# Optimization experiments

Hardware: AMD Instinct MI355X
Metric: run time of the kernel (lower is better)

## Reference

```python
import jax, jax.numpy as jnp
import numpy as np

N, E = 16384, 262144
IN, H, OUT = 128, 256, 256
L, HEADS = 4, 8
OC = H // HEADS  # 32, also MHA head_dim
B, NB = 64, 256  # graphs, nodes per graph (N = B*NB, equal-size graphs)


def _ln(x, g, b, eps=1e-5):
    m = x.mean(-1, keepdims=True)
    v = ((x - m) ** 2).mean(-1, keepdims=True)
    return (x - m) / jnp.sqrt(v + eps) * g + b


def setup_inputs() -> dict:
    key = jax.random.key(0)
    ks = iter(jax.random.split(key, 40))
    r = lambda *s: jax.random.normal(next(ks), s, jnp.float32) * 0.05
    return dict(
        x=jax.random.normal(next(ks), (N, IN), jnp.float32),
        edge_index=jax.random.randint(next(ks), (2, E), 0, N),
        wi=r(IN, H), bi=r(H),
        wg=r(L, H, H), asrc=r(L, HEADS, OC), adst=r(L, HEADS, OC), bg=r(L, H),
        g1=jnp.ones((L, H)), b1=jnp.zeros((L, H)),
        inw=r(L, 3 * H, H), inb=r(L, 3 * H), ow=r(L, H, H), ob=r(L, H),
        g2=jnp.ones((L, H)), b2=jnp.zeros((L, H)),
        mw1=r(L, H, 2 * H), mb1=r(L, 2 * H), mw2=r(L, 2 * H, H), mb2=r(L, H),
        g3=jnp.ones((L, H)), b3=jnp.zeros((L, H)),
        gf=jnp.ones(H), bf=jnp.zeros(H),
        wo=r(H, OUT), bo=r(OUT),
    )


def reference(x, edge_index, wi, bi, wg, asrc, adst, bg, g1, b1, inw, inb,
              ow, ob, g2, b2, mw1, mb1, mw2, mb2, g3, b3, gf, bf, wo, bo):
    src, dst = edge_index[0], edge_index[1]
    x = jax.nn.relu(x @ wi + bi)  # [N, H]
    for i in range(L):
        # ---- GATConv (local MPNN), eval mode (no dropout) ----
        xw = (x @ wg[i]).reshape(N, HEADS, OC)
        a = (xw * asrc[i]).sum(-1)[src] + (xw * adst[i]).sum(-1)[dst]  # [E, HEADS]
        a = jax.nn.leaky_relu(a, 0.2)
        amax = jax.ops.segment_max(a, dst, num_segments=N)
        ae = jnp.exp(a - amax[dst])
        asum = jax.ops.segment_sum(ae, dst, num_segments=N)
        attn = ae / asum[dst]  # edge softmax per destination node
        h = jax.ops.segment_sum(attn[:, :, None] * xw[src], dst, num_segments=N)
        h = h.reshape(N, H) + bg[i]
        h = _ln(h + x, g1[i], b1[i])  # GPSConv local branch + residual + norm1
        # ---- global MultiheadAttention over dense batch (equal-size graphs) ----
        xd = x.reshape(B, NB, H)
        qkv = xd @ inw[i].T + inb[i]
        q, k, v = jnp.split(qkv, 3, axis=-1)
        q = q.reshape(B, NB, HEADS, OC).transpose(0, 2, 1, 3)
        k = k.reshape(B, NB, HEADS, OC).transpose(0, 2, 1, 3)
        v = v.reshape(B, NB, HEADS, OC).transpose(0, 2, 1, 3)
        p = jax.nn.softmax(jnp.einsum('bhqd,bhkd->bhqk', q, k) / jnp.sqrt(jnp.float32(OC)), axis=-1)
        o = jnp.einsum('bhqk,bhkd->bhqd', p, v).transpose(0, 2, 1, 3).reshape(B, NB, H)
        o = (o @ ow[i].T + ob[i]).reshape(N, H)
        h2 = _ln(o + x, g2[i], b2[i])  # global branch + residual + norm2
        out = h + h2
        out = out + (jax.nn.relu(out @ mw1[i] + mb1[i]) @ mw2[i] + mb2[i])  # MLP residual
        x = _ln(out, g3[i], b3[i])  # norm3
    x = _ln(x, gf, bf)
    return x @ wo + bo
```

## Files before the change

### kernel.cpp

```cpp
#include <hip/hip_runtime.h>
#include <hip/hip_bf16.h>

#define NNODES 16384
#define NEDGES 262144
#define IND    128
#define HD     256
#define OUTDIM 256
#define LAYERS 4
#define NHEADS 8
#define OCD    32
#define NGRAPH 64
#define NBATCH 256
#define XQSTR  1024

typedef __hip_bfloat16 bf16;
typedef __attribute__((ext_vector_type(8))) short bf16x8;
typedef __attribute__((ext_vector_type(4))) short s16x4;
typedef __attribute__((ext_vector_type(4))) float f32x4;

__device__ __forceinline__ short bfbits(float v) {
    bf16 h = __float2bfloat16(v);
    return *(short*)&h;
}
__device__ __forceinline__ float b2f(short s) {
    return __uint_as_float(((unsigned)(unsigned short)s) << 16);
}

__device__ __forceinline__ void gload_lds16(const short* g, short* l) {
    __builtin_amdgcn_global_load_lds(
        (const __attribute__((address_space(1))) void*)g,
        (__attribute__((address_space(3))) void*)l, 16, 0, 0);
}

__global__ void cvt_kernel(const float* __restrict__ in, short* __restrict__ out, int n)
{
    int i = blockIdx.x * blockDim.x + threadIdx.x;
    if (i < n) out[i] = bfbits(in[i]);
}

__global__ void transpose_cvt_kernel(const float* __restrict__ in, short* __restrict__ out,
                                     int K, int N)
{
    int i = blockIdx.x * blockDim.x + threadIdx.x;
    if (i >= K * N) return;
    const float* ip = in + (size_t)blockIdx.y * K * N;
    short* op = out + (size_t)blockIdx.y * K * N;
    int k = i / N, n = i % N;
    op[(size_t)n * K + k] = bfbits(ip[i]);
}

__global__ void build_wcomb_kernel(const float* __restrict__ inw, const float* __restrict__ wg,
                                   short* __restrict__ wcomb)
{
    int i = blockIdx.x * blockDim.x + threadIdx.x;
    int l = i >> 18, r = (i >> 8) & 1023, k = i & 255;
    float v;
    if (r < 768) v = inw[(size_t)l * 768 * 256 + r * 256 + k];
    else         v = wg[(size_t)l * 256 * 256 + k * 256 + (r - 768)];
    wcomb[i] = bfbits(v);
}

__global__ void build_cbias_kernel(const float* __restrict__ inb, float* __restrict__ cbias)
{
    int i = blockIdx.x * blockDim.x + threadIdx.x;
    int l = i >> 10, c = i & 1023;
    cbias[i] = (c < 768) ? inb[l * 768 + c] : 0.f;
}

__global__ void hist_kernel(const int* __restrict__ dst, int* __restrict__ cnt)
{
    int e = blockIdx.x * blockDim.x + threadIdx.x;
    if (e < NEDGES) atomicAdd(&cnt[dst[e]], 1);
}

__global__ void scan_kernel(const int* __restrict__ cnt, int* __restrict__ row_ptr)
{
    __shared__ int part[256];
    int t = threadIdx.x;
    const int PER = NNODES / 256;
    int base = t * PER;
    int s = 0;
    for (int i = 0; i < PER; i++) s += cnt[base + i];
    part[t] = s;
    __syncthreads();
    for (int off = 1; off < 256; off <<= 1) {
        int v = (t >= off) ? part[t - off] : 0;
        __syncthreads();
        part[t] += v;
        __syncthreads();
    }
    int run = (t == 0) ? 0 : part[t - 1];
    for (int i = 0; i < PER; i++) { row_ptr[base + i] = run; run += cnt[base + i]; }
    if (t == 255) row_ptr[NNODES] = run;
}

__global__ void scatter_kernel(const int* __restrict__ src, const int* __restrict__ dst,
                               const int* __restrict__ row_ptr, int* __restrict__ fill,
                               int* __restrict__ srcs)
{
    int e = blockIdx.x * blockDim.x + threadIdx.x;
    if (e >= NEDGES) return;
    int d = dst[e];
    int pos = row_ptr[d] + atomicAdd(&fill[d], 1);
    srcs[pos] = src[e];
}

__global__ void gat_scores_kernel(const short* __restrict__ xw16,
                                  const float* __restrict__ asrc, const float* __restrict__ adst,
                                  float* __restrict__ ssrc, float* __restrict__ sdst)
{
    int i = blockIdx.x * blockDim.x + threadIdx.x;
    if (i >= NNODES * NHEADS) return;
    int n = i >> 3, h = i & 7;
    const bf16x8* xr = (const bf16x8*)(xw16 + (size_t)n * XQSTR + h * OCD);
    float s1 = 0.f, s2 = 0.f;
#pragma unroll
    for (int g = 0; g < 4; g++) {
        bf16x8 v8 = xr[g];
#pragma unroll
        for (int j = 0; j < 8; j++) {
            float v = b2f(v8[j]);
            int d = g * 8 + j;
            s1 += v * asrc[h * OCD + d];
            s2 += v * adst[h * OCD + d];
        }
    }
    ssrc[i] = s1;
    sdst[i] = s2;
}

__global__ __launch_bounds__(256)
void gat_agg_ln_kernel(const int* __restrict__ row_ptr, const int* __restrict__ srcs,
                       const float* __restrict__ ssrc, const float* __restrict__ sdst,
                       const short* __restrict__ xw16, const float* __restrict__ xcur,
                       const float* __restrict__ colbias, const float* __restrict__ gamma,
                       const float* __restrict__ beta, float* __restrict__ out)
{
    int wave = threadIdx.x >> 6, lane = threadIdx.x & 63;
    int n = blockIdx.x * 4 + wave;
    int c0 = lane << 2;
    int h = c0 >> 5;
    int start = row_ptr[n];
    int deg = row_ptr[n + 1] - start;
    float sd = sdst[n * NHEADS + h];

    float ax = 0.f, ay = 0.f, az = 0.f, aw = 0.f, l = 0.f;
    int j = 0;
    for (; j + 4 <= deg; j += 4) {
        int e0 = srcs[start + j + 0], e1 = srcs[start + j + 1];
        int e2 = srcs[start + j + 2], e3 = srcs[start + j + 3];
        s16x4 r0 = *(const s16x4*)&xw16[(size_t)e0 * XQSTR + c0];
        s16x4 r1 = *(const s16x4*)&xw16[(size_t)e1 * XQSTR + c0];
        s16x4 r2 = *(const s16x4*)&xw16[(size_t)e2 * XQSTR + c0];
        s16x4 r3 = *(const s16x4*)&xw16[(size_t)e3 * XQSTR + c0];
        float a0 = ssrc[e0 * NHEADS + h] + sd; a0 = a0 > 0.f ? a0 : 0.2f * a0;
        float a1 = ssrc[e1 * NHEADS + h] + sd; a1 = a1 > 0.f ? a1 : 0.2f * a1;
        float a2 = ssrc[e2 * NHEADS + h] + sd; a2 = a2 > 0.f ? a2 : 0.2f * a2;
        float a3 = ssrc[e3 * NHEADS + h] + sd; a3 = a3 > 0.f ? a3 : 0.2f * a3;
        float p0 = __expf(a0), p1 = __expf(a1), p2 = __expf(a2), p3 = __expf(a3);
        l += (p0 + p1) + (p2 + p3);
        ax += p0 * b2f(r0[0]) + p1 * b2f(r1[0]) + p2 * b2f(r2[0]) + p3 * b2f(r3[0]);
        ay += p0 * b2f(r0[1]) + p1 * b2f(r1[1]) + p2 * b2f(r2[1]) + p3 * b2f(r3[1]);
        az += p0 * b2f(r0[2]) + p1 * b2f(r1[2]) + p2 * b2f(r2[2]) + p3 * b2f(r3[2]);
        aw += p0 * b2f(r0[3]) + p1 * b2f(r1[3]) + p2 * b2f(r2[3]) + p3 * b2f(r3[3]);
    }
    for (; j < deg; j++) {
        int e0 = srcs[start + j];
        s16x4 r0 = *(const s16x4*)&xw16[(size_t)e0 * XQSTR + c0];
        float a0 = ssrc[e0 * NHEADS + h] + sd; a0 = a0 > 0.f ? a0 : 0.2f * a0;
        float p0 = __expf(a0);
        l += p0;
        ax += p0 * b2f(r0[0]); ay += p0 * b2f(r0[1]);
        az += p0 * b2f(r0[2]); aw += p0 * b2f(r0[3]);
    }
    float invl = deg ? 1.f / l : 0.f;
    size_t base = (size_t)n * HD + c0;
    float4 x4 = *(const float4*)&xcur[base];
    float4 cb = *(const float4*)&colbias[c0];
    float4 v;
    v.x = ax * invl + x4.x + cb.x;
    v.y = ay * invl + x4.y + cb.y;
    v.z = az * invl + x4.z + cb.z;
    v.w = aw * invl + x4.w + cb.w;
    float s = v.x + v.y + v.z + v.w;
    float q = v.x * v.x + v.y * v.y + v.z * v.z + v.w * v.w;
#pragma unroll
    for (int off = 1; off < 64; off <<= 1) {
        s += __shfl_xor(s, off);
        q += __shfl_xor(q, off);
    }
    float mean = s * (1.f / HD);
    float var  = fmaxf(q * (1.f / HD) - mean * mean, 0.f);
    float inv  = rsqrtf(var + 1e-5f);
    float4 g  = *(const float4*)&gamma[c0];
    float4 bt = *(const float4*)&beta[c0];
    float4 y;
    y.x = (v.x - mean) * inv * g.x + bt.x;
    y.y = (v.y - mean) * inv * g.y + bt.y;
    y.z = (v.z - mean) * inv * g.z + bt.z;
    y.w = (v.w - mean) * inv * g.w + bt.w;
    *(float4*)&out[base] = y;
}

#define GBM 128
#define GBK 32

template<int TN>
__global__ __launch_bounds__(256)
void gemm_mfma_kernel(const short* __restrict__ A16, const short* __restrict__ B16,
                      const float* __restrict__ bias, const float* __restrict__ resid,
                      float* __restrict__ Cf, short* __restrict__ C16,
                      int M, int Nc, int K, int relu)
{
    constexpr int NTF = TN / 32;
    __shared__ short As[GBM * GBK];
    __shared__ short Bs[TN * GBK];
    int tid = threadIdx.x;
    int wid = tid >> 6, lane = tid & 63;
    int quad = lane >> 4, l16 = lane & 15;
    int wm = wid >> 1, wn = wid & 1;
    int rowBase = blockIdx.y * GBM;
    int colBase = blockIdx.x * TN;

    f32x4 acc[4][NTF];
#pragma unroll
    for (int mt = 0; mt < 4; mt++)
#pragma unroll
        for (int nt = 0; nt < NTF; nt++) acc[mt][nt] = (f32x4)(0.f);

    int ar  = tid >> 2;
    int akq = (tid & 3) * 8;

    const short* Ag0 = &A16[(size_t)(rowBase + ar) * K + akq];
    const short* Ag1 = &A16[(size_t)(rowBase + ar + 64) * K + akq];
    const short* Bg0 = &B16[(size_t)(colBase + ar) * K + akq];
    const short* Bg1 = (TN == 128) ? &B16[(size_t)(colBase + ar + 64) * K + akq] : nullptr;
    short* AsW0 = As + wid * 512;
    short* AsW1 = As + 64 * GBK + wid * 512;
    short* BsW0 = Bs + wid * 512;
    short* BsW1 = Bs + 64 * GBK + wid * 512;

    for (int k0 = 0; k0 < K; k0 += GBK) {
        gload_lds16(Ag0 + k0, AsW0);
        gload_lds16(Ag1 + k0, AsW1);
        gload_lds16(Bg0 + k0, BsW0);
        if (TN == 128) gload_lds16(Bg1 + k0, BsW1);
        __syncthreads();
        bf16x8 aF[4], bF[NTF];
#pragma unroll
        for (int mt = 0; mt < 4; mt++)
            aF[mt] = *(bf16x8*)&As[(wm * 64 + mt * 16 + l16) * GBK + quad * 8];
#pragma unroll
        for (int nt = 0; nt < NTF; nt++)
            bF[nt] = *(bf16x8*)&Bs[(wn * (TN / 2) + nt * 16 + l16) * GBK + quad * 8];
#pragma unroll
        for (int mt = 0; mt < 4; mt++)
#pragma unroll
            for (int nt = 0; nt < NTF; nt++)
                acc[mt][nt] = __builtin_amdgcn_mfma_f32_16x16x32_bf16(
                    bF[nt], aF[mt], acc[mt][nt], 0, 0, 0);
        __syncthreads();
    }

#pragma unroll
    for (int mt = 0; mt < 4; mt++) {
        int row = rowBase + wm * 64 + mt * 16 + l16;
#pragma unroll
        for (int nt = 0; nt < NTF; nt++) {
            int col0 = colBase + wn * (TN / 2) + nt * 16 + quad * 4;
            f32x4 v = acc[mt][nt];
            if (bias) {
                float4 b4 = *(const float4*)&bias[col0];
                v[0] += b4.x; v[1] += b4.y; v[2] += b4.z; v[3] += b4.w;
            }
            if (resid) {
                float4 r4 = *(const float4*)&resid[(size_t)row * Nc + col0];
                v[0] += r4.x; v[1] += r4.y; v[2] += r4.z; v[3] += r4.w;
            }
            if (relu) {
                v[0] = fmaxf(v[0], 0.f); v[1] = fmaxf(v[1], 0.f);
                v[2] = fmaxf(v[2], 0.f); v[3] = fmaxf(v[3], 0.f);
            }
            if (Cf) {
                float4 o; o.x = v[0]; o.y = v[1]; o.z = v[2]; o.w = v[3];
                *(float4*)&Cf[(size_t)row * Nc + col0] = o;
            }
            if (C16) {
                s16x4 o;
                o[0] = bfbits(v[0]); o[1] = bfbits(v[1]);
                o[2] = bfbits(v[2]); o[3] = bfbits(v[3]);
                *(s16x4*)&C16[(size_t)row * Nc + col0] = o;
            }
        }
    }
}

__global__ __launch_bounds__(256)
void gemm_ln_kernel(const short* __restrict__ A16, const short* __restrict__ B16,
                    const float* __restrict__ bias, const float* __restrict__ resid,
                    const float* __restrict__ gamma, const float* __restrict__ beta,
                    const float* __restrict__ postadd,
                    float* __restrict__ outf, short* __restrict__ out16, int K)
{
    __shared__ short As[GBM * GBK];
    __shared__ short Bs[256 * GBK];
    __shared__ float sred_s[2][GBM];
    __shared__ float sred_q[2][GBM];
    int tid = threadIdx.x;
    int wid = tid >> 6, lane = tid & 63;
    int quad = lane >> 4, l16 = lane & 15;
    int wm = wid >> 1, wn = wid & 1;
    int rowBase = blockIdx.y * GBM;

    f32x4 acc[4][8];
#pragma unroll
    for (int mt = 0; mt < 4; mt++)
#pragma unroll
        for (int nt = 0; nt < 8; nt++) acc[mt][nt] = (f32x4)(0.f);

    int ar  = tid >> 2;
    int akq = (tid & 3) * 8;

    const short* Ag0 = &A16[(size_t)(rowBase + ar) * K + akq];
    const short* Ag1 = &A16[(size_t)(rowBase + ar + 64) * K + akq];
    const short* Bg0 = &B16[(size_t)(ar) * K + akq];
    const short* Bg1 = &B16[(size_t)(ar + 64) * K + akq];
    const short* Bg2 = &B16[(size_t)(ar + 128) * K + akq];
    const short* Bg3 = &B16[(size_t)(ar + 192) * K + akq];
    short* AsW0 = As + wid * 512;
    short* AsW1 = As + 64 * GBK + wid * 512;
    short* BsW0 = Bs + wid * 512;
    short* BsW1 = Bs + 64 * GBK + wid * 512;
    short* BsW2 = Bs + 128 * GBK + wid * 512;
    short* BsW3 = Bs + 192 * GBK + wid * 512;

    for (int k0 = 0; k0 < K; k0 += GBK) {
        gload_lds16(Ag0 + k0, AsW0);
        gload_lds16(Ag1 + k0, AsW1);
        gload_lds16(Bg0 + k0, BsW0);
        gload_lds16(Bg1 + k0, BsW1);
        gload_lds16(Bg2 + k0, BsW2);
        gload_lds16(Bg3 + k0, BsW3);
        __syncthreads();
        bf16x8 aF[4], bF[8];
#pragma unroll
        for (int mt = 0; mt < 4; mt++)
            aF[mt] = *(bf16x8*)&As[(wm * 64 + mt * 16 + l16) * GBK + quad * 8];
#pragma unroll
        for (int nt = 0; nt < 8; nt++)
            bF[nt] = *(bf16x8*)&Bs[(wn * 128 + nt * 16 + l16) * GBK + quad * 8];
#pragma unroll
        for (int mt = 0; mt < 4; mt++)
#pragma unroll
            for (int nt = 0; nt < 8; nt++)
                acc[mt][nt] = __builtin_amdgcn_mfma_f32_16x16x32_bf16(
                    bF[nt], aF[mt], acc[mt][nt], 0, 0, 0);
        __syncthreads();
    }

#pragma unroll
    for (int mt = 0; mt < 4; mt++) {
        int row = rowBase + wm * 64 + mt * 16 + l16;
        float s = 0.f, q = 0.f;
#pragma unroll
        for (int nt = 0; nt < 8; nt++) {
            int col0 = wn * 128 + nt * 16 + quad * 4;
            f32x4 v = acc[mt][nt];
            float4 b4 = *(const float4*)&bias[col0];
            float4 r4 = *(const float4*)&resid[(size_t)row * HD + col0];
            v[0] += b4.x + r4.x; v[1] += b4.y + r4.y;
            v[2] += b4.z + r4.z; v[3] += b4.w + r4.w;
            acc[mt][nt] = v;
            s += (v[0] + v[1]) + (v[2] + v[3]);
            q += (v[0] * v[0] + v[1] * v[1]) + (v[2] * v[2] + v[3] * v[3]);
        }
        s += __shfl_xor(s, 16); s += __shfl_xor(s, 32);
        q += __shfl_xor(q, 16); q += __shfl_xor(q, 32);
        if (quad == 0) {
            sred_s[wn][wm * 64 + mt * 16 + l16] = s;
            sred_q[wn][wm * 64 + mt * 16 + l16] = q;
        }
    }
    __syncthreads();
#pragma unroll
    for (int mt = 0; mt < 4; mt++) {
        int rowl = wm * 64 + mt * 16 + l16;
        int row = rowBase + rowl;
        float s = sred_s[0][rowl] + sred_s[1][rowl];
        float q = sred_q[0][rowl] + sred_q[1][rowl];
        float mean = s * (1.f / HD);
        float var  = fmaxf(q * (1.f / HD) - mean * mean, 0.f);
        float inv  = rsqrtf(var + 1e-5f);
#pragma unroll
        for (int nt = 0; nt < 8; nt++) {
            int col0 = wn * 128 + nt * 16 + quad * 4;
            f32x4 v = acc[mt][nt];
            float4 g4 = *(const float4*)&gamma[col0];
            float4 bt = *(const float4*)&beta[col0];
            float4 y;
            y.x = (v[0] - mean) * inv * g4.x + bt.x;
            y.y = (v[1] - mean) * inv * g4.y + bt.y;
            y.z = (v[2] - mean) * inv * g4.z + bt.z;
            y.w = (v[3] - mean) * inv * g4.w + bt.w;
            if (postadd) {
                float4 p4 = *(const float4*)&postadd[(size_t)row * HD + col0];
                y.x += p4.x; y.y += p4.y; y.z += p4.z; y.w += p4.w;
            }
            *(float4*)&outf[(size_t)row * HD + col0] = y;
            s16x4 o;
            o[0] = bfbits(y.x); o[1] = bfbits(y.y); o[2] = bfbits(y.z); o[3] = bfbits(y.w);
            *(s16x4*)&out16[(size_t)row * HD + col0] = o;
        }
    }
}

__global__ __launch_bounds__(256)
void ln4_kernel(const float* __restrict__ in, const float* __restrict__ res,
                const float* __restrict__ gamma, const float* __restrict__ beta,
                const float* __restrict__ postadd,
                float* __restrict__ outf, short* __restrict__ out16)
{
    int wave = threadIdx.x >> 6, lane = threadIdx.x & 63;
    int row = blockIdx.x * 4 + wave;
    size_t base = (size_t)row * HD + lane * 4;
    float4 v = *(const float4*)&in[base];
    if (res) {
        float4 r = *(const float4*)&res[base];
        v.x += r.x; v.y += r.y; v.z += r.z; v.w += r.w;
    }
    float s = v.x + v.y + v.z + v.w;
    float q = v.x * v.x + v.y * v.y + v.z * v.z + v.w * v.w;
#pragma unroll
    for (int off = 1; off < 64; off <<= 1) {
        s += __shfl_xor(s, off);
        q += __shfl_xor(q, off);
    }
    float mean = s * (1.f / HD);
    float var  = fmaxf(q * (1.f / HD) - mean * mean, 0.f);
    float inv  = rsqrtf(var + 1e-5f);
    float4 g  = *(const float4*)&gamma[lane * 4];
    float4 bt = *(const float4*)&beta[lane * 4];
    float4 y;
    y.x = (v.x - mean) * inv * g.x + bt.x;
    y.y = (v.y - mean) * inv * g.y + bt.y;
    y.z = (v.z - mean) * inv * g.z + bt.z;
    y.w = (v.w - mean) * inv * g.w + bt.w;
    if (postadd) {
        float4 p = *(const float4*)&postadd[base];
        y.x += p.x; y.y += p.y; y.z += p.z; y.w += p.w;
    }
    if (outf) *(float4*)&outf[base] = y;
    if (out16) {
        s16x4 o;
        o[0] = bfbits(y.x); o[1] = bfbits(y.y); o[2] = bfbits(y.z); o[3] = bfbits(y.w);
        *(s16x4*)&out16[base] = o;
    }
}

#define PSTR 72
__global__ __launch_bounds__(256)
void mha_mfma_kernel(const short* __restrict__ qkv16, short* __restrict__ o16)
{
    __shared__ short smem[4 * 64 * PSTR + 32 * PSTR];
    short* VT = smem + 4 * 64 * PSTR;

    int b = blockIdx.x, h = blockIdx.y;
    int tid = threadIdx.x;
    int wid = tid >> 6, lane = tid & 63;
    int quad = lane >> 4, l16 = lane & 15;
    int base = b * NBATCH;
    int qrow0 = wid * 64;
    short* Pme = smem + wid * 64 * PSTR;

    const float scale2 = 0.17677669529663687f * 1.4426950408889634f;

    bf16x8 qA[4];
#pragma unroll
    for (int mt = 0; mt < 4; mt++)
        qA[mt] = *(const bf16x8*)&qkv16[(size_t)(base + qrow0 + mt * 16 + l16) * XQSTR + h * 32 + quad * 8];

    f32x4 accO[4][2];
#pragma unroll
    for (int mt = 0; mt < 4; mt++)
#pragma unroll
        for (int dt = 0; dt < 2; dt++) accO[mt][dt] = (f32x4)(0.f);
    float lsum[4][4];
#pragma unroll
    for (int mt = 0; mt < 4; mt++)
#pragma unroll
        for (int r = 0; r < 4; r++) lsum[mt][r] = 0.f;

    for (int c = 0; c < 4; c++) {
        __syncthreads();
        {
            int key = tid >> 2, dq = (tid & 3) * 8;
            bf16x8 v = *(const bf16x8*)&qkv16[(size_t)(base + c * 64 + key) * XQSTR + 512 + h * 32 + dq];
#pragma unroll
            for (int j = 0; j < 8; j++) VT[(dq + j) * PSTR + key] = v[j];
        }
        __syncthreads();
        bf16x8 kB[4];
#pragma unroll
        for (int kt = 0; kt < 4; kt++)
            kB[kt] = *(const bf16x8*)&qkv16[(size_t)(base + c * 64 + kt * 16 + l16) * XQSTR + 256 + h * 32 + quad * 8];
#pragma unroll
        for (int mt = 0; mt < 4; mt++) {
#pragma unroll
            for (int kt = 0; kt < 4; kt++) {
                f32x4 s = __builtin_amdgcn_mfma_f32_16x16x32_bf16(qA[mt], kB[kt], (f32x4)(0.f), 0, 0, 0);
#pragma unroll
                for (int r = 0; r < 4; r++) {
                    float p = exp2f(s[r] * scale2);
                    lsum[mt][r] += p;
                    Pme[(mt * 16 + quad * 4 + r) * PSTR + kt * 16 + l16] = bfbits(p);
                }
            }
        }
        __syncthreads();
#pragma unroll
        for (int mt = 0; mt < 4; mt++) {
#pragma unroll
            for (int ks = 0; ks < 2; ks++) {
                bf16x8 pA = *(bf16x8*)&Pme[(mt * 16 + l16) * PSTR + ks * 32 + quad * 8];
#pragma unroll
                for (int dt = 0; dt < 2; dt++) {
                    bf16x8 vB = *(bf16x8*)&VT[(dt * 16 + l16) * PSTR + ks * 32 + quad * 8];
                    accO[mt][dt] = __builtin_amdgcn_mfma_f32_16x16x32_bf16(pA, vB, accO[mt][dt], 0, 0, 0);
                }
            }
        }
    }
#pragma unroll
    for (int mt = 0; mt < 4; mt++)
#pragma unroll
        for (int r = 0; r < 4; r++) {
            float v = lsum[mt][r];
            v += __shfl_xor(v, 1);
            v += __shfl_xor(v, 2);
            v += __shfl_xor(v, 4);
            v += __shfl_xor(v, 8);
            lsum[mt][r] = v;
        }
#pragma unroll
    for (int mt = 0; mt < 4; mt++)
#pragma unroll
        for (int dt = 0; dt < 2; dt++)
#pragma unroll
            for (int r = 0; r < 4; r++) {
                int row = base + qrow0 + mt * 16 + quad * 4 + r;
                int col = h * 32 + dt * 16 + l16;
                o16[(size_t)row * HD + col] = bfbits(accO[mt][dt][r] / lsum[mt][r]);
            }
}

extern "C" void kernel_launch(void* const* d_in, const int* in_sizes, int n_in,
                              void* d_out, int out_size, void* d_ws, size_t ws_size,
                              hipStream_t stream)
{
    const float* x0   = (const float*)d_in[0];
    const int*   ei   = (const int*)d_in[1];
    const float* wi   = (const float*)d_in[2];
    const float* bi   = (const float*)d_in[3];
    const float* wg   = (const float*)d_in[4];
    const float* asrc = (const float*)d_in[5];
    const float* adst = (const float*)d_in[6];
    const float* bg   = (const float*)d_in[7];
    const float* g1   = (const float*)d_in[8];
    const float* b1   = (const float*)d_in[9];
    const float* inw  = (const float*)d_in[10];
    const float* inb  = (const float*)d_in[11];
    const float* ow   = (const float*)d_in[12];
    const float* ob   = (const float*)d_in[13];
    const float* g2   = (const float*)d_in[14];
    const float* b2   = (const float*)d_in[15];
    const float* mw1  = (const float*)d_in[16];
    const float* mb1  = (const float*)d_in[17];
    const float* mw2  = (const float*)d_in[18];
    const float* mb2  = (const float*)d_in[19];
    const float* g3   = (const float*)d_in[20];
    const float* b3   = (const float*)d_in[21];
    const float* gf   = (const float*)d_in[22];
    const float* bf_  = (const float*)d_in[23];
    const float* wo   = (const float*)d_in[24];
    const float* bo   = (const float*)d_in[25];

    const int* srcI = ei;
    const int* dstI = ei + NEDGES;

    const size_t NH = (size_t)NNODES * HD;
    float* ws   = (float*)d_ws;
    float* xcur = ws;
    float* xw   = xcur + NH;
    float* hbuf = xw + NH;
    float* obuf = hbuf + NH;
    float* qkvb = obuf + NH;
    int*   srcs    = (int*)(qkvb + 3 * NH);
    int*   row_ptr = srcs + NEDGES;
    int*   cnt     = row_ptr + NNODES + 1;
    int*   fill    = cnt + NNODES;
    float* ssrc    = (float*)(fill + NNODES);
    float* sdst    = ssrc + (size_t)NNODES * NHEADS;
    short* xq16   = (short*)qkvb;
    short* x016   = (short*)(sdst + (size_t)NNODES * NHEADS);
    short* xcur16 = x016 + (size_t)NNODES * IND;
    short* b16a   = xcur16 + NH;
    short* hid16  = b16a + NH;
    short* wi_t  = hid16 + 2 * NH;
    short* wcomb = wi_t + (size_t)HD * IND;
    short* ow_c  = wcomb + (size_t)LAYERS * 1024 * HD;
    short* mw1_t = ow_c + (size_t)LAYERS * HD * HD;
    short* mw2_t = mw1_t + (size_t)LAYERS * HD * 2 * HD;
    short* wo_t  = mw2_t + (size_t)LAYERS * 2 * HD * HD;
    float* cbias = (float*)(wo_t + (size_t)HD * OUTDIM);

    const int T = 256;
    const int nNH = NNODES * NHEADS;

    cvt_kernel<<<(NNODES * IND + T - 1) / T, T, 0, stream>>>(x0, x016, NNODES * IND);
    transpose_cvt_kernel<<<dim3((IND * HD + T - 1) / T, 1), T, 0, stream>>>(wi, wi_t, IND, HD);
    build_wcomb_kernel<<<(LAYERS * 1024 * HD) / T, T, 0, stream>>>(inw, wg, wcomb);
    build_cbias_kernel<<<(LAYERS * 1024) / T, T, 0, stream>>>(inb, cbias);
    cvt_kernel<<<(LAYERS * HD * HD + T - 1) / T, T, 0, stream>>>(ow, ow_c, LAYERS * HD * HD);
    transpose_cvt_kernel<<<dim3((HD * 2 * HD + T - 1) / T, LAYERS), T, 0, stream>>>(mw1, mw1_t, HD, 2 * HD);
    transpose_cvt_kernel<<<dim3((2 * HD * HD + T - 1) / T, LAYERS), T, 0, stream>>>(mw2, mw2_t, 2 * HD, HD);
    transpose_cvt_kernel<<<dim3((HD * OUTDIM + T - 1) / T, 1), T, 0, stream>>>(wo, wo_t, HD, OUTDIM);

    hipMemsetAsync(cnt, 0, NNODES * sizeof(int), stream);
    hipMemsetAsync(fill, 0, NNODES * sizeof(int), stream);
    hist_kernel<<<(NEDGES + T - 1) / T, T, 0, stream>>>(dstI, cnt);
    scan_kernel<<<1, 256, 0, stream>>>(cnt, row_ptr);
    scatter_kernel<<<(NEDGES + T - 1) / T, T, 0, stream>>>(srcI, dstI, row_ptr, fill, srcs);

    gemm_mfma_kernel<64><<<dim3(HD / 64, NNODES / GBM), 256, 0, stream>>>(
        x016, wi_t, bi, nullptr, xcur, xcur16, NNODES, HD, IND, 1);

    for (int i = 0; i < LAYERS; i++) {
        const float* asrc_i = asrc + (size_t)i * NHEADS * OCD;
        const float* adst_i = adst + (size_t)i * NHEADS * OCD;
        const float* bg_i   = bg + (size_t)i * HD;
        const float* g1_i   = g1 + (size_t)i * HD;
        const float* b1_i   = b1 + (size_t)i * HD;
        const float* ob_i   = ob + (size_t)i * HD;
        const float* g2_i   = g2 + (size_t)i * HD;
        const float* b2_i   = b2 + (size_t)i * HD;
        const float* mb1_i  = mb1 + (size_t)i * 2 * HD;
        const float* mb2_i  = mb2 + (size_t)i * HD;
        const float* g3_i   = g3 + (size_t)i * HD;
        const float* b3_i   = b3 + (size_t)i * HD;
        const short* wcomb_i = wcomb + (size_t)i * 1024 * HD;
        const float* cbias_i = cbias + (size_t)i * 1024;
        const short* ow_ci  = ow_c + (size_t)i * HD * HD;
        const short* mw1_ti = mw1_t + (size_t)i * HD * 2 * HD;
        const short* mw2_ti = mw2_t + (size_t)i * 2 * HD * HD;

        gemm_mfma_kernel<128><<<dim3(1024 / 128, NNODES / GBM), 256, 0, stream>>>(
            xcur16, wcomb_i, cbias_i, nullptr, nullptr, xq16, NNODES, 1024, HD, 0);

        gat_scores_kernel<<<(nNH + T - 1) / T, T, 0, stream>>>(xq16 + 768, asrc_i, adst_i, ssrc, sdst);
        gat_agg_ln_kernel<<<NNODES / 4, 256, 0, stream>>>(
            row_ptr, srcs, ssrc, sdst, xq16 + 768, xcur, bg_i, g1_i, b1_i, hbuf);

        mha_mfma_kernel<<<dim3(NGRAPH, NHEADS), 256, 0, stream>>>(xq16, b16a);
        gemm_ln_kernel<<<dim3(1, NNODES / GBM), 256, 0, stream>>>(
            b16a, ow_ci, ob_i, xcur, g2_i, b2_i, hbuf, obuf, b16a, HD);

        gemm_mfma_kernel<128><<<dim3(2 * HD / 128, NNODES / GBM), 256, 0, stream>>>(
            b16a, mw1_ti, mb1_i, nullptr, nullptr, hid16, NNODES, 2 * HD, HD, 1);
        gemm_ln_kernel<<<dim3(1, NNODES / GBM), 256, 0, stream>>>(
            hid16, mw2_ti, mb2_i, obuf, g3_i, b3_i, nullptr, xcur, xcur16, 2 * HD);
    }

    ln4_kernel<<<NNODES / 4, 256, 0, stream>>>(xcur, nullptr, gf, bf_, nullptr, nullptr, b16a);
    gemm_mfma_kernel<64><<<dim3(OUTDIM / 64, NNODES / GBM), 256, 0, stream>>>(
        b16a, wo_t, bo, nullptr, (float*)d_out, nullptr, NNODES, OUTDIM, HD, 0);
}
```

Baseline: 892.7 us.

## Shrink gemm_ln row tile to 64 and fuse weight prep into one kernel

The GEMM+LayerNorm kernel now uses 64-row tiles in which each wave owns 16 full rows across all 256 columns. Row statistics are reduced within a wave by shuffles, so the shared-memory reduction and its extra barrier go away, and the grid doubles from 128 to 256 blocks for better CU occupancy. The separate conversion, transpose and memset launches are also merged into a single prep kernel to cut launch overhead. The trade-off is less B-tile reuse per block, since each block reloads the whole weight matrix for half as many rows.

```diff
diff --git a/kernel.cpp b/kernel.cpp
--- a/kernel.cpp
+++ b/kernel.cpp
@@ -32,39 +32,67 @@
         (__attribute__((address_space(3))) void*)l, 16, 0, 0);
 }
 
-__global__ void cvt_kernel(const float* __restrict__ in, short* __restrict__ out, int n)
+#define PREP_TOTAL (32768 + NNODES*IND + IND*HD + LAYERS*1024*HD + LAYERS*1024 \
+                    + LAYERS*HD*HD + LAYERS*HD*2*HD + LAYERS*2*HD*HD + HD*OUTDIM)
+__global__ void prep_kernel(const float* __restrict__ x0, const float* __restrict__ wi,
+                            const float* __restrict__ inw, const float* __restrict__ wg,
+                            const float* __restrict__ inb, const float* __restrict__ ow,
+                            const float* __restrict__ mw1, const float* __restrict__ mw2,
+                            const float* __restrict__ wo,
+                            short* __restrict__ x016, short* __restrict__ wi_t,
+                            short* __restrict__ wcomb, float* __restrict__ cbias,
+                            short* __restrict__ ow_c, short* __restrict__ mw1_t,
+                            short* __restrict__ mw2_t, short* __restrict__ wo_t,
+                            int* __restrict__ cnt, int* __restrict__ fill)
 {
     int i = blockIdx.x * blockDim.x + threadIdx.x;
-    if (i < n) out[i] = bfbits(in[i]);
-}
-
-__global__ void transpose_cvt_kernel(const float* __restrict__ in, short* __restrict__ out,
-                                     int K, int N)
-{
-    int i = blockIdx.x * blockDim.x + threadIdx.x;
-    if (i >= K * N) return;
-    const float* ip = in + (size_t)blockIdx.y * K * N;
-    short* op = out + (size_t)blockIdx.y * K * N;
-    int k = i / N, n = i % N;
-    op[(size_t)n * K + k] = bfbits(ip[i]);
-}
-
-__global__ void build_wcomb_kernel(const float* __restrict__ inw, const float* __restrict__ wg,
-                                   short* __restrict__ wcomb)
-{
-    int i = blockIdx.x * blockDim.x + threadIdx.x;
-    int l = i >> 18, r = (i >> 8) & 1023, k = i & 255;
-    float v;
-    if (r < 768) v = inw[(size_t)l * 768 * 256 + r * 256 + k];
-    else         v = wg[(size_t)l * 256 * 256 + k * 256 + (r - 768)];
-    wcomb[i] = bfbits(v);
-}
-
-__global__ void build_cbias_kernel(const float* __restrict__ inb, float* __restrict__ cbias)
-{
-    int i = blockIdx.x * blockDim.x + threadIdx.x;
-    int l = i >> 10, c = i & 1023;
-    cbias[i] = (c < 768) ? inb[l * 768 + c] : 0.f;
+    if (i < 32768) {
+        if (i < NNODES) cnt[i] = 0; else fill[i - NNODES] = 0;
+        return;
+    }
+    i -= 32768;
+    if (i < NNODES * IND) { x016[i] = bfbits(x0[i]); return; }
+    i -= NNODES * IND;
+    if (i < IND * HD) {
+        int k = i / HD, n = i % HD;
+        wi_t[n * IND + k] = bfbits(wi[i]);
+        return;
+    }
+    i -= IND * HD;
+    if (i < LAYERS * 1024 * HD) {
+        int l = i >> 18, r = (i >> 8) & 1023, k = i & 255;
+        float v = (r < 768) ? inw[(size_t)l * 768 * 256 + r * 256 + k]
+                            : wg[(size_t)l * 256 * 256 + k * 256 + (r - 768)];
+        wcomb[i] = bfbits(v);
+        return;
+    }
+    i -= LAYERS * 1024 * HD;
+    if (i < LAYERS * 1024) {
+        int l = i >> 10, c = i & 1023;
+        cbias[i] = (c < 768) ? inb[l * 768 + c] : 0.f;
+        return;
+    }
+    i -= LAYERS * 1024;
+    if (i < LAYERS * HD * HD) { ow_c[i] = bfbits(ow[i]); return; }
+    i -= LAYERS * HD * HD;
+    if (i < LAYERS * HD * 2 * HD) {
+        int l = i / (HD * 2 * HD), r = i % (HD * 2 * HD);
+        int k = r / (2 * HD), n = r % (2 * HD);
+        mw1_t[(size_t)l * HD * 2 * HD + n * HD + k] = bfbits(mw1[i]);
+        return;
+    }
+    i -= LAYERS * HD * 2 * HD;
+    if (i < LAYERS * 2 * HD * HD) {
+        int l = i / (2 * HD * HD), r = i % (2 * HD * HD);
+        int k = r / HD, n = r % HD;
+        mw2_t[(size_t)l * 2 * HD * HD + n * 2 * HD + k] = bfbits(mw2[i]);
+        return;
+    }
+    i -= LAYERS * 2 * HD * HD;
+    if (i < HD * OUTDIM) {
+        int k = i / OUTDIM, n = i % OUTDIM;
+        wo_t[n * HD + k] = bfbits(wo[i]);
+    }
 }
 
 __global__ void hist_kernel(const int* __restrict__ dst, int* __restrict__ cnt)
@@ -302,115 +330,85 @@
                     const float* __restrict__ postadd,
                     float* __restrict__ outf, short* __restrict__ out16, int K)
 {
-    __shared__ short As[GBM * GBK];
+    __shared__ short As[64 * GBK];
     __shared__ short Bs[256 * GBK];
-    __shared__ float sred_s[2][GBM];
-    __shared__ float sred_q[2][GBM];
     int tid = threadIdx.x;
     int wid = tid >> 6, lane = tid & 63;
     int quad = lane >> 4, l16 = lane & 15;
-    int wm = wid >> 1, wn = wid & 1;
-    int rowBase = blockIdx.y * GBM;
-
-    f32x4 acc[4][8];
-#pragma unroll
-    for (int mt = 0; mt < 4; mt++)
-#pragma unroll
-        for (int nt = 0; nt < 8; nt++) acc[mt][nt] = (f32x4)(0.f);
+    int rowBase = blockIdx.y * 64;
+
+    f32x4 acc[16];
+#pragma unroll
+    for (int nt = 0; nt < 16; nt++) acc[nt] = (f32x4)(0.f);
 
     int ar  = tid >> 2;
     int akq = (tid & 3) * 8;
 
-    const short* Ag0 = &A16[(size_t)(rowBase + ar) * K + akq];
-    const short* Ag1 = &A16[(size_t)(rowBase + ar + 64) * K + akq];
+    const short* Ag  = &A16[(size_t)(rowBase + ar) * K + akq];
     const short* Bg0 = &B16[(size_t)(ar) * K + akq];
     const short* Bg1 = &B16[(size_t)(ar + 64) * K + akq];
     const short* Bg2 = &B16[(size_t)(ar + 128) * K + akq];
     const short* Bg3 = &B16[(size_t)(ar + 192) * K + akq];
-    short* AsW0 = As + wid * 512;
-    short* AsW1 = As + 64 * GBK + wid * 512;
+    short* AsW  = As + wid * 512;
     short* BsW0 = Bs + wid * 512;
     short* BsW1 = Bs + 64 * GBK + wid * 512;
     short* BsW2 = Bs + 128 * GBK + wid * 512;
     short* BsW3 = Bs + 192 * GBK + wid * 512;
 
     for (int k0 = 0; k0 < K; k0 += GBK) {
-        gload_lds16(Ag0 + k0, AsW0);
-        gload_lds16(Ag1 + k0, AsW1);
+        gload_lds16(Ag + k0, AsW);
         gload_lds16(Bg0 + k0, BsW0);
         gload_lds16(Bg1 + k0, BsW1);
         gload_lds16(Bg2 + k0, BsW2);
         gload_lds16(Bg3 + k0, BsW3);
         __syncthreads();
-        bf16x8 aF[4], bF[8];
-#pragma unroll
-        for (int mt = 0; mt < 4; mt++)
-            aF[mt] = *(bf16x8*)&As[(wm * 64 + mt * 16 + l16) * GBK + quad * 8];
-#pragma unroll
-        for (int nt = 0; nt < 8; nt++)
-            bF[nt] = *(bf16x8*)&Bs[(wn * 128 + nt * 16 + l16) * GBK + quad * 8];
-#pragma unroll
-        for (int mt = 0; mt < 4; mt++)
-#pragma unroll
-            for (int nt = 0; nt < 8; nt++)
-                acc[mt][nt] = __builtin_amdgcn_mfma_f32_16x16x32_bf16(
-                    bF[nt], aF[mt], acc[mt][nt], 0, 0, 0);
-        __syncthreads();
-    }
-
-#pragma unroll
-    for (int mt = 0; mt < 4; mt++) {
-        int row = rowBase + wm * 64 + mt * 16 + l16;
-        float s = 0.f, q = 0.f;
-#pragma unroll
-        for (int nt = 0; nt < 8; nt++) {
-            int col0 = wn * 128 + nt * 16 + quad * 4;
-            f32x4 v = acc[mt][nt];
-            float4 b4 = *(const float4*)&bias[col0];
-            float4 r4 = *(const float4*)&resid[(size_t)row * HD + col0];
-            v[0] += b4.x + r4.x; v[1] += b4.y + r4.y;
-            v[2] += b4.z + r4.z; v[3] += b4.w + r4.w;
-            acc[mt][nt] = v;
-            s += (v[0] + v[1]) + (v[2] + v[3]);
-            q += (v[0] * v[0] + v[1] * v[1]) + (v[2] * v[2] + v[3] * v[3]);
-        }
-        s += __shfl_xor(s, 16); s += __shfl_xor(s, 32);
-        q += __shfl_xor(q, 16); q += __shfl_xor(q, 32);
-        if (quad == 0) {
-            sred_s[wn][wm * 64 + mt * 16 + l16] = s;
-            sred_q[wn][wm * 64 + mt * 16 + l16] = q;
-        }
-    }
-    __syncthreads();
-#pragma unroll
-    for (int mt = 0; mt < 4; mt++) {
-        int rowl = wm * 64 + mt * 16 + l16;
-        int row = rowBase + rowl;
-        float s = sred_s[0][rowl] + sred_s[1][rowl];
-        float q = sred_q[0][rowl] + sred_q[1][rowl];
-        float mean = s * (1.f / HD);
-        float var  = fmaxf(q * (1.f / HD) - mean * mean, 0.f);
-        float inv  = rsqrtf(var + 1e-5f);
-#pragma unroll
-        for (int nt = 0; nt < 8; nt++) {
-            int col0 = wn * 128 + nt * 16 + quad * 4;
-            f32x4 v = acc[mt][nt];
-            float4 g4 = *(const float4*)&gamma[col0];
-            float4 bt = *(const float4*)&beta[col0];
-            float4 y;
-            y.x = (v[0] - mean) * inv * g4.x + bt.x;
-            y.y = (v[1] - mean) * inv * g4.y + bt.y;
-            y.z = (v[2] - mean) * inv * g4.z + bt.z;
-            y.w = (v[3] - mean) * inv * g4.w + bt.w;
-            if (postadd) {
-                float4 p4 = *(const float4*)&postadd[(size_t)row * HD + col0];
-                y.x += p4.x; y.y += p4.y; y.z += p4.z; y.w += p4.w;
-            }
-            *(float4*)&outf[(size_t)row * HD + col0] = y;
-            s16x4 o;
-            o[0] = bfbits(y.x); o[1] = bfbits(y.y); o[2] = bfbits(y.z); o[3] = bfbits(y.w);
-            *(s16x4*)&out16[(size_t)row * HD + col0] = o;
-        }
+        bf16x8 aF = *(bf16x8*)&As[(wid * 16 + l16) * GBK + quad * 8];
+#pragma unroll
+        for (int nt = 0; nt < 16; nt++) {
+            bf16x8 bF = *(bf16x8*)&Bs[(nt * 16 + l16) * GBK + quad * 8];
+            acc[nt] = __builtin_amdgcn_mfma_f32_16x16x32_bf16(bF, aF, acc[nt], 0, 0, 0);
+        }
+        __syncthreads();
+    }
+
+    int row = rowBase + wid * 16 + l16;
+    float s = 0.f, q = 0.f;
+#pragma unroll
+    for (int nt = 0; nt < 16; nt++) {
+        int col0 = nt * 16 + quad * 4;
+        f32x4 v = acc[nt];
+        float4 b4 = *(const float4*)&bias[col0];
+        float4 r4 = *(const float4*)&resid[(size_t)row * HD + col0];
+        v[0] += b4.x + r4.x; v[1] += b4.y + r4.y;
+        v[2] += b4.z + r4.z; v[3] += b4.w + r4.w;
+        acc[nt] = v;
+        s += (v[0] + v[1]) + (v[2] + v[3]);
+        q += (v[0] * v[0] + v[1] * v[1]) + (v[2] * v[2] + v[3] * v[3]);
+    }
+    s += __shfl_xor(s, 16); s += __shfl_xor(s, 32);
+    q += __shfl_xor(q, 16); q += __shfl_xor(q, 32);
+    float mean = s * (1.f / HD);
+    float var  = fmaxf(q * (1.f / HD) - mean * mean, 0.f);
+    float inv  = rsqrtf(var + 1e-5f);
+#pragma unroll
+    for (int nt = 0; nt < 16; nt++) {
+        int col0 = nt * 16 + quad * 4;
+        f32x4 v = acc[nt];
+        float4 g4 = *(const float4*)&gamma[col0];
+        float4 bt = *(const float4*)&beta[col0];
+        float4 y;
+        y.x = (v[0] - mean) * inv * g4.x + bt.x;
+        y.y = (v[1] - mean) * inv * g4.y + bt.y;
+        y.z = (v[2] - mean) * inv * g4.z + bt.z;
+        y.w = (v[3] - mean) * inv * g4.w + bt.w;
+        if (postadd) {
+            float4 p4 = *(const float4*)&postadd[(size_t)row * HD + col0];
+            y.x += p4.x; y.y += p4.y; y.z += p4.z; y.w += p4.w;
+        }
+        *(float4*)&outf[(size_t)row * HD + col0] = y;
+        s16x4 o;
+        o[0] = bfbits(y.x); o[1] = bfbits(y.y); o[2] = bfbits(y.z); o[3] = bfbits(y.w);
+        *(s16x4*)&out16[(size_t)row * HD + col0] = o;
     }
 }
 
@@ -616,17 +614,10 @@
     const int T = 256;
     const int nNH = NNODES * NHEADS;
 
-    cvt_kernel<<<(NNODES * IND + T - 1) / T, T, 0, stream>>>(x0, x016, NNODES * IND);
-    transpose_cvt_kernel<<<dim3((IND * HD + T - 1) / T, 1), T, 0, stream>>>(wi, wi_t, IND, HD);
-    build_wcomb_kernel<<<(LAYERS * 1024 * HD) / T, T, 0, stream>>>(inw, wg, wcomb);
-    build_cbias_kernel<<<(LAYERS * 1024) / T, T, 0, stream>>>(inb, cbias);
-    cvt_kernel<<<(LAYERS * HD * HD + T - 1) / T, T, 0, stream>>>(ow, ow_c, LAYERS * HD * HD);
-    transpose_cvt_kernel<<<dim3((HD * 2 * HD + T - 1) / T, LAYERS), T, 0, stream>>>(mw1, mw1_t, HD, 2 * HD);
-    transpose_cvt_kernel<<<dim3((2 * HD * HD + T - 1) / T, LAYERS), T, 0, stream>>>(mw2, mw2_t, 2 * HD, HD);
-    transpose_cvt_kernel<<<dim3((HD * OUTDIM + T - 1) / T, 1), T, 0, stream>>>(wo, wo_t, HD, OUTDIM);
-
-    hipMemsetAsync(cnt, 0, NNODES * sizeof(int), stream);
-    hipMemsetAsync(fill, 0, NNODES * sizeof(int), stream);
+    prep_kernel<<<(PREP_TOTAL + T - 1) / T, T, 0, stream>>>(
+        x0, wi, inw, wg, inb, ow, mw1, mw2, wo,
+        x016, wi_t, wcomb, cbias, ow_c, mw1_t, mw2_t, wo_t, cnt, fill);
+
     hist_kernel<<<(NEDGES + T - 1) / T, T, 0, stream>>>(dstI, cnt);
     scan_kernel<<<1, 256, 0, stream>>>(cnt, row_ptr);
     scatter_kernel<<<(NEDGES + T - 1) / T, T, 0, stream>>>(srcI, dstI, row_ptr, fill, srcs);
@@ -661,12 +652,12 @@
             row_ptr, srcs, ssrc, sdst, xq16 + 768, xcur, bg_i, g1_i, b1_i, hbuf);
 
         mha_mfma_kernel<<<dim3(NGRAPH, NHEADS), 256, 0, stream>>>(xq16, b16a);
-        gemm_ln_kernel<<<dim3(1, NNODES / GBM), 256, 0, stream>>>(
+        gemm_ln_kernel<<<dim3(1, NNODES / 64), 256, 0, stream>>>(
             b16a, ow_ci, ob_i, xcur, g2_i, b2_i, hbuf, obuf, b16a, HD);
 
         gemm_mfma_kernel<128><<<dim3(2 * HD / 128, NNODES / GBM), 256, 0, stream>>>(
             b16a, mw1_ti, mb1_i, nullptr, nullptr, hid16, NNODES, 2 * HD, HD, 1);
-        gemm_ln_kernel<<<dim3(1, NNODES / GBM), 256, 0, stream>>>(
+        gemm_ln_kernel<<<dim3(1, NNODES / 64), 256, 0, stream>>>(
             hid16, mw2_ti, mb2_i, obuf, g3_i, b3_i, nullptr, xcur, xcur16, 2 * HD);
     }
 
```

After: 814.2 us. 1.1x faster.
